# Kernel optimization log

Measured on AMD Instinct MI355X. Metric: run time of the kernel, lower is better.

The kernel has to match this reference:

```python
import jax, jax.numpy as jnp
import numpy as np

N = 100_000      # nodes
E = 500_000      # bonds
DN = 128         # dim_node_embedding
DB = 64          # dim_bond_embedding
NTOK = 4         # num_bond_token
DIN = 2 * DN + 2 * DB  # 384
LEAKY = 0.001
LN_EPS = 1e-5
DIST_MAX = 20.0
STEP = 0.5


def _lrelu(v):
    return jnp.where(v >= 0, v, LEAKY * v)


def _layernorm(v, w, b):
    m = v.mean(-1, keepdims=True)
    var = ((v - m) ** 2).mean(-1, keepdims=True)
    return (v - m) / jnp.sqrt(var + LN_EPS) * w + b


def setup_inputs() -> dict:
    key = jax.random.key(0)
    ks = jax.random.split(key, 20)
    x = jax.random.normal(ks[0], (N, 3), dtype=jnp.float32) * 3.0
    pos = jax.random.normal(ks[1], (N, 3), dtype=jnp.float32)
    node_embedding = jax.random.normal(ks[2], (N, DN), dtype=jnp.float32)
    i0 = jax.random.randint(ks[3], (E,), 0, N)
    off = jax.random.randint(ks[4], (E,), 1, N)  # nonzero -> no self-bonds
    bond_index = jnp.stack([i0, (i0 + off) % N], axis=1).astype(jnp.int32)
    bond_types = jax.random.randint(ks[5], (E,), 0, NTOK).astype(jnp.int32)
    s = 0.02
    params = dict(
        bond_emb=jax.random.normal(ks[6], (NTOK, DB), dtype=jnp.float32),
        W0=jax.random.normal(ks[7], (DIN, DN), dtype=jnp.float32) * s,
        b0=jnp.zeros((DN,), jnp.float32),
        W1=jax.random.normal(ks[8], (DN, DN), dtype=jnp.float32) * s,
        b1=jnp.zeros((DN,), jnp.float32),
        ln1_w=jnp.ones((DN,), jnp.float32),
        ln1_b=jnp.zeros((DN,), jnp.float32),
        W2=jax.random.normal(ks[9], (DN, DN), dtype=jnp.float32) * s,
        b2=jnp.zeros((DN,), jnp.float32),
        ln2_w=jnp.ones((DN,), jnp.float32),
        ln2_b=jnp.zeros((DN,), jnp.float32),
        Wo=jax.random.normal(ks[10], (DN, 2), dtype=jnp.float32) * s,
        bo=jnp.zeros((2,), jnp.float32),
    )
    return dict(x=x, pos=pos, node_embedding=node_embedding,
                bond_index=bond_index, bond_types=bond_types, **params)


def reference(x, pos, node_embedding, bond_index, bond_types,
              bond_emb, W0, b0, W1, b1, ln1_w, ln1_b,
              W2, b2, ln2_w, ln2_b, Wo, bo):
    i = bond_index[:, 0]
    j = bond_index[:, 1]

    # ---- BondLength geometry ----
    diff = x[i] - x[j]                                   # [E,3]
    dist = jnp.linalg.norm(diff, axis=-1, keepdims=True)  # [E,1]
    u = diff / dist                                       # [E,3] unit j->i? (i-j)/d
    direction = jnp.stack([u, -u], axis=-1)               # [E,3,2]

    # ---- Smearing (gaussian RBF + overflow bin, normalized) ----
    offset = jnp.linspace(0.0, DIST_MAX, DB - 1, dtype=jnp.float32)  # [63]
    delta = DIST_MAX / (DB - 2)
    coeff = -0.5 / (delta * delta)
    rbf = jnp.exp(coeff * (dist - offset) ** 2)            # [E,63]
    ovf = (dist >= DIST_MAX).astype(x.dtype)               # [E,1]
    smear = jnp.concatenate([rbf, ovf], axis=-1)           # [E,64]
    smear = smear / smear.sum(axis=-1, keepdims=True)

    # ---- Edge MLP (LeakyMLP, num_layer=2, dim_end=2) ----
    feat = jnp.concatenate(
        [node_embedding[i], node_embedding[j], bond_emb[bond_types], smear],
        axis=-1)                                           # [E,384]
    h = _lrelu(feat @ W0 + b0)
    h = _lrelu(_layernorm(h @ W1 + b1, ln1_w, ln1_b))
    h = _lrelu(_layernorm(h @ W2 + b2, ln2_w, ln2_b))
    force = h @ Wo + bo                                    # [E,2]

    # ---- position update (scatter-add) ----
    update = force[:, None, :] * direction                 # [E,3,2]
    pos = pos.at[i].add(STEP * update[..., 0])
    pos = pos.at[j].add(STEP * update[..., 1])
    return pos
```

## Files before the change

### kernel.cpp

```cpp
#include <hip/hip_runtime.h>
#include <stdint.h>

#define N_EDGES 500000
#define N_NODES 100000
#define PREP_NG 2
#define TBINS 1280

typedef __attribute__((ext_vector_type(8))) short short8;
typedef __attribute__((ext_vector_type(4))) float floatx4;

__device__ __forceinline__ uint16_t f2bf(float f) {
  union { float f; uint32_t u; } cv; cv.f = f;
  uint32_t u = cv.u;
  return (uint16_t)((u + 0x7FFFu + ((u >> 16) & 1u)) >> 16);
}
__device__ __forceinline__ uint32_t pk2bf(float lo, float hi) {
  return __builtin_amdgcn_perm(__float_as_uint(hi), __float_as_uint(lo), 0x07060302u);
}
__device__ __forceinline__ uint16_t bftrunc(float f) {
  return (uint16_t)(__float_as_uint(f) >> 16);
}
__device__ __forceinline__ float bf2f_lo(uint32_t u) { return __uint_as_float(u << 16); }
__device__ __forceinline__ float bf2f_hi(uint32_t u) { return __uint_as_float(u & 0xFFFF0000u); }
__device__ __forceinline__ float lrelu(float v) { return fmaxf(v, 0.001f * v); }

__global__ void prep0_kernel(const float* __restrict__ W0, const float* __restrict__ b0,
                             const float* __restrict__ W1, const float* __restrict__ W2,
                             const float* __restrict__ bemb,
                             uint16_t* __restrict__ w0ab, uint16_t* __restrict__ w1f,
                             uint16_t* __restrict__ w2f, float* __restrict__ be0f,
                             const float* __restrict__ pos, float* __restrict__ out, int npos) {
  int id = blockIdx.x * 256 + threadIdx.x;
  if (id < 32768) {
    int f = id;
    int j = f & 7, lane = (f >> 3) & 63, ntt = (f >> 9) & 15, ks = f >> 13;
    int k = ks * 32 + (lane >> 4) * 8 + j;
    int row = (ntt < 8) ? k : (128 + k);
    int col = (ntt & 7) * 16 + (lane & 15);
    w0ab[f] = f2bf(W0[row * 128 + col]);
  } else if (id < 49152) {
    int f = id - 32768;
    int j = f & 7, lane = (f >> 3) & 63, nt = (f >> 9) & 7, ks = f >> 12;
    int k = ks * 32 + (lane >> 4) * 8 + j;
    w1f[f] = f2bf(W1[k * 128 + nt * 16 + (lane & 15)]);
  } else if (id < 65536) {
    int f = id - 49152;
    int j = f & 7, lane = (f >> 3) & 63, nt = (f >> 9) & 7, ks = f >> 12;
    int k = ks * 32 + (lane >> 4) * 8 + j;
    w2f[f] = f2bf(W2[k * 128 + nt * 16 + (lane & 15)]);
  } else if (id < 66048) {
    int t = id - 65536; int ty = t >> 7, n = t & 127;
    float s = b0[n];
    for (int kk = 0; kk < 64; ++kk) s += bemb[ty * 64 + kk] * W0[(256 + kk) * 128 + n];
    be0f[t] = s;
  } else if (id - 66048 < npos) {
    out[id - 66048] = pos[id - 66048];
  }
}

__global__ void prep_t_kernel(const float* __restrict__ W0, const float* __restrict__ be0f,
                              uint16_t* __restrict__ T) {
  int id = blockIdx.x * 256 + threadIdx.x;
  if (id >= 4 * TBINS * 128) return;
  int n = id & 127;
  int tb = id >> 7;
  int b = tb % TBINS;
  int ty = tb / TBINS;
  float dist = (float)b * (1.0f / 32.0f);
  const float delta = 20.0f / 62.0f;
  const float coeff = -0.5f / (delta * delta);
  float sum = 0.0f;
  for (int k = 0; k < 63; ++k) { float d = dist - (float)k * delta; sum += __expf(coeff * d * d); }
  float ovf = (dist >= 20.0f) ? 1.0f : 0.0f;
  sum += ovf;
  float rs = 1.0f / sum;
  float s = be0f[ty * 128 + n];
  for (int k = 0; k < 63; ++k) {
    float d = dist - (float)k * delta;
    s += __expf(coeff * d * d) * rs * W0[(320 + k) * 128 + n];
  }
  s += ovf * rs * W0[(320 + 63) * 128 + n];
  T[id] = f2bf(s);
}

__global__ __attribute__((amdgpu_flat_work_group_size(256, 256), amdgpu_waves_per_eu(1, 4)))
void prep_p_kernel(const float* __restrict__ nemb, const uint16_t* __restrict__ w0ab,
                   uint16_t* __restrict__ Pa, uint16_t* __restrict__ Pb) {
  __shared__ __align__(16) uint16_t aLds[4 * PREP_NG * 16 * 136];
  const int tid = threadIdx.x;
  const int lane = tid & 63;
  const int wave = tid >> 6;
  const int n15 = lane & 15;
  const int quad = lane >> 4;
  uint16_t* myA = aLds + wave * (PREP_NG * 16 * 136);
  const int base = blockIdx.x * (64 * PREP_NG) + wave * (16 * PREP_NG);

  {
    const int le = lane >> 2, sub = lane & 3;
#pragma unroll
    for (int it = 0; it < PREP_NG; ++it) {
      int r = base + it * 16 + le; if (r >= N_NODES) r = N_NODES - 1;
      const float4* src = (const float4*)(nemb + (size_t)r * 128);
#pragma unroll
      for (int g = 0; g < 4; ++g) {
        float4 a = src[sub * 8 + g * 2], b = src[sub * 8 + g * 2 + 1];
        uint4 pk;
        pk.x = pk2bf(a.x, a.y); pk.y = pk2bf(a.z, a.w);
        pk.z = pk2bf(b.x, b.y); pk.w = pk2bf(b.z, b.w);
        *(uint4*)(myA + (it * 16 + le) * 136 + sub * 32 + g * 8) = pk;
      }
    }
  }

  const short8* wfv = (const short8*)w0ab + lane;
#pragma unroll
  for (int q = 0; q < 4; ++q) {
    short8 bfr[16];
#pragma unroll
    for (int ks = 0; ks < 4; ++ks)
#pragma unroll
      for (int nq = 0; nq < 4; ++nq)
        bfr[ks * 4 + nq] = wfv[(ks * 16 + q * 4 + nq) * 64];
#pragma unroll
    for (int it = 0; it < PREP_NG; ++it) {
      floatx4 acc[4];
#pragma unroll
      for (int nq = 0; nq < 4; ++nq) acc[nq] = (floatx4){0.f, 0.f, 0.f, 0.f};
#pragma unroll
      for (int ks = 0; ks < 4; ++ks) {
        short8 a = *(const short8*)(myA + (it * 16 + n15) * 136 + ks * 32 + quad * 8);
#pragma unroll
        for (int nq = 0; nq < 4; ++nq)
          acc[nq] = __builtin_amdgcn_mfma_f32_16x16x32_bf16(a, bfr[ks * 4 + nq], acc[nq], 0, 0, 0);
      }
      uint16_t* dst = (q < 2) ? Pa : Pb;
      int cbase = ((q & 1) * 4) * 16 + n15;
#pragma unroll
      for (int nq = 0; nq < 4; ++nq) {
        int c = cbase + nq * 16;
#pragma unroll
        for (int r = 0; r < 4; ++r) {
          int row = base + it * 16 + quad * 4 + r;
          if (row < N_NODES) dst[(size_t)row * 128 + c] = bftrunc(acc[nq][r]);
        }
      }
    }
  }
}

template <int NKS>
__device__ __forceinline__ void gemm2(const uint16_t* __restrict__ wf,
                                      const uint16_t* aR0, const uint16_t* aR1,
                                      int lane, floatx4* acc0, floatx4* acc1) {
  const short8* wfv = (const short8*)wf + lane;
  short8 a0[NKS], a1[NKS];
#pragma unroll
  for (int ks = 0; ks < NKS; ++ks) {
    a0[ks] = *(const short8*)(aR0 + ks * 32);
    a1[ks] = *(const short8*)(aR1 + ks * 32);
  }
#pragma unroll
  for (int ks = 0; ks < NKS; ++ks)
#pragma unroll
    for (int nt = 0; nt < 8; ++nt) {
      short8 b = wfv[(ks * 8 + nt) * 64];
      acc0[nt] = __builtin_amdgcn_mfma_f32_16x16x32_bf16(a0[ks], b, acc0[nt], 0, 0, 0);
      acc1[nt] = __builtin_amdgcn_mfma_f32_16x16x32_bf16(a1[ks], b, acc1[nt], 0, 0, 0);
    }
}

__global__ __attribute__((amdgpu_flat_work_group_size(256, 256)))
void bond_mlp_kernel(const float* __restrict__ x,
                     const int* __restrict__ bidx, const int* __restrict__ btyp,
                     const uint16_t* __restrict__ Pa, const uint16_t* __restrict__ Pb,
                     const uint16_t* __restrict__ Tt, const uint16_t* __restrict__ w1f,
                     const uint16_t* __restrict__ w2f,
                     const float* __restrict__ b1, const float* __restrict__ ln1w,
                     const float* __restrict__ ln1b,
                     const float* __restrict__ b2, const float* __restrict__ ln2w,
                     const float* __restrict__ ln2b,
                     const float* __restrict__ Wo, const float* __restrict__ bo,
                     float* __restrict__ out) {
  __shared__ __align__(16) uint16_t hA_all[4 * 32 * 136];
  __shared__ float u_lds[128][3];
  __shared__ int ij_lds[128][2];

  const int tid = threadIdx.x;
  const int lane = tid & 63;
  const int wave = tid >> 6;
  const int n15 = lane & 15;
  const int quad = lane >> 4;

  uint16_t* hA = hA_all + wave * (32 * 136);

#pragma unroll
  for (int p = 0; p < 2; ++p) {
    const int le = lane >> 2, sub = lane & 3;
    const int row = p * 16 + le;
    const int gr = wave * 32 + row;
    const int ge = blockIdx.x * 128 + gr;
    const bool valid = ge < N_EDGES;
    int vi = 0, vj = 0, bt = 0;
    if (valid) { vi = bidx[2 * ge]; vj = bidx[2 * ge + 1]; bt = btyp[ge]; }
    float dx, dy, dz;
    if (valid) {
      dx = x[3 * vi]     - x[3 * vj];
      dy = x[3 * vi + 1] - x[3 * vj + 1];
      dz = x[3 * vi + 2] - x[3 * vj + 2];
    } else { dx = 1.0f; dy = 0.0f; dz = 0.0f; }
    float dist = sqrtf(dx * dx + dy * dy + dz * dz);
    float rinv = 1.0f / dist;
    if (sub == 0) {
      u_lds[gr][0] = dx * rinv; u_lds[gr][1] = dy * rinv; u_lds[gr][2] = dz * rinv;
      ij_lds[gr][0] = vi; ij_lds[gr][1] = vj;
    }
    float fb = fminf(dist, 39.5f) * 32.0f;
    int bi = (int)fb;
    float w = fb - (float)bi;
    const uint4* pa = (const uint4*)(Pa + (size_t)vi * 128 + sub * 32);
    const uint4* pb = (const uint4*)(Pb + (size_t)vj * 128 + sub * 32);
    const uint16_t* trow = Tt + ((size_t)(bt * TBINS + bi)) * 128 + sub * 32;
    const uint4* t0p = (const uint4*)trow;
    const uint4* t1p = (const uint4*)(trow + 128);
#pragma unroll
    for (int g = 0; g < 4; ++g) {
      uint4 av = pa[g], bv = pb[g], t0 = t0p[g], t1 = t1p[g];
      uint4 pk;
      {
        float lo = bf2f_lo(av.x) + bf2f_lo(bv.x), hi = bf2f_hi(av.x) + bf2f_hi(bv.x);
        float l0 = bf2f_lo(t0.x), l1 = bf2f_lo(t1.x), h0 = bf2f_hi(t0.x), h1 = bf2f_hi(t1.x);
        pk.x = pk2bf(lrelu(lo + l0 + w * (l1 - l0)), lrelu(hi + h0 + w * (h1 - h0)));
      }
      {
        float lo = bf2f_lo(av.y) + bf2f_lo(bv.y), hi = bf2f_hi(av.y) + bf2f_hi(bv.y);
        float l0 = bf2f_lo(t0.y), l1 = bf2f_lo(t1.y), h0 = bf2f_hi(t0.y), h1 = bf2f_hi(t1.y);
        pk.y = pk2bf(lrelu(lo + l0 + w * (l1 - l0)), lrelu(hi + h0 + w * (h1 - h0)));
      }
      {
        float lo = bf2f_lo(av.z) + bf2f_lo(bv.z), hi = bf2f_hi(av.z) + bf2f_hi(bv.z);
        float l0 = bf2f_lo(t0.z), l1 = bf2f_lo(t1.z), h0 = bf2f_hi(t0.z), h1 = bf2f_hi(t1.z);
        pk.z = pk2bf(lrelu(lo + l0 + w * (l1 - l0)), lrelu(hi + h0 + w * (h1 - h0)));
      }
      {
        float lo = bf2f_lo(av.w) + bf2f_lo(bv.w), hi = bf2f_hi(av.w) + bf2f_hi(bv.w);
        float l0 = bf2f_lo(t0.w), l1 = bf2f_lo(t1.w), h0 = bf2f_hi(t0.w), h1 = bf2f_hi(t1.w);
        pk.w = pk2bf(lrelu(lo + l0 + w * (l1 - l0)), lrelu(hi + h0 + w * (h1 - h0)));
      }
      *(uint4*)(hA + row * 136 + sub * 32 + g * 8) = pk;
    }
  }

  const uint16_t* aR0 = hA + n15 * 136 + quad * 8;
  const uint16_t* aR1 = hA + (16 + n15) * 136 + quad * 8;

  floatx4 acc0[8], acc1[8];
#pragma unroll
  for (int nt = 0; nt < 8; ++nt) {
    acc0[nt] = (floatx4){0.f, 0.f, 0.f, 0.f};
    acc1[nt] = (floatx4){0.f, 0.f, 0.f, 0.f};
  }
  gemm2<4>(w1f, aR0, aR1, lane, acc0, acc1);

  {
    float bv[8], wv[8], bb2[8];
#pragma unroll
    for (int nt = 0; nt < 8; ++nt) {
      int col = nt * 16 + n15;
      bv[nt] = b1[col]; wv[nt] = ln1w[col]; bb2[nt] = ln1b[col];
    }
#pragma unroll
    for (int t = 0; t < 2; ++t) {
      floatx4* acc = t ? acc1 : acc0;
      float s[4] = {0,0,0,0}, q[4] = {0,0,0,0};
#pragma unroll
      for (int nt = 0; nt < 8; ++nt)
#pragma unroll
        for (int r = 0; r < 4; ++r) { float v = acc[nt][r] + bv[nt]; s[r] += v; q[r] += v * v; }
#pragma unroll
      for (int m = 1; m <= 8; m <<= 1)
#pragma unroll
        for (int r = 0; r < 4; ++r) { s[r] += __shfl_xor(s[r], m); q[r] += __shfl_xor(q[r], m); }
      float mean[4], rstd[4];
#pragma unroll
      for (int r = 0; r < 4; ++r) {
        mean[r] = s[r] * (1.0f / 128.0f);
        float var = q[r] * (1.0f / 128.0f) - mean[r] * mean[r];
        rstd[r] = rsqrtf(var + 1e-5f);
      }
#pragma unroll
      for (int nt = 0; nt < 8; ++nt)
#pragma unroll
        for (int r = 0; r < 4; ++r) {
          float v = acc[nt][r] + bv[nt];
          float vn = (v - mean[r]) * rstd[r] * wv[nt] + bb2[nt];
          hA[(t * 16 + quad * 4 + r) * 136 + nt * 16 + n15] = bftrunc(lrelu(vn));
        }
    }
  }

#pragma unroll
  for (int nt = 0; nt < 8; ++nt) {
    acc0[nt] = (floatx4){0.f, 0.f, 0.f, 0.f};
    acc1[nt] = (floatx4){0.f, 0.f, 0.f, 0.f};
  }
  gemm2<4>(w2f, aR0, aR1, lane, acc0, acc1);

  {
    float bv[8], wv[8], bb2[8], wo0[8], wo1[8];
#pragma unroll
    for (int nt = 0; nt < 8; ++nt) {
      int col = nt * 16 + n15;
      bv[nt] = b2[col]; wv[nt] = ln2w[col]; bb2[nt] = ln2b[col];
      wo0[nt] = Wo[2 * col]; wo1[nt] = Wo[2 * col + 1];
    }
    float bo0 = bo[0], bo1 = bo[1];
#pragma unroll
    for (int t = 0; t < 2; ++t) {
      floatx4* acc = t ? acc1 : acc0;
      float s[4] = {0,0,0,0}, q[4] = {0,0,0,0};
#pragma unroll
      for (int nt = 0; nt < 8; ++nt)
#pragma unroll
        for (int r = 0; r < 4; ++r) { float v = acc[nt][r] + bv[nt]; s[r] += v; q[r] += v * v; }
#pragma unroll
      for (int m = 1; m <= 8; m <<= 1)
#pragma unroll
        for (int r = 0; r < 4; ++r) { s[r] += __shfl_xor(s[r], m); q[r] += __shfl_xor(q[r], m); }
      float mean[4], rstd[4];
#pragma unroll
      for (int r = 0; r < 4; ++r) {
        mean[r] = s[r] * (1.0f / 128.0f);
        float var = q[r] * (1.0f / 128.0f) - mean[r] * mean[r];
        rstd[r] = rsqrtf(var + 1e-5f);
      }
      float f0[4] = {0,0,0,0}, f1[4] = {0,0,0,0};
#pragma unroll
      for (int nt = 0; nt < 8; ++nt)
#pragma unroll
        for (int r = 0; r < 4; ++r) {
          float v = acc[nt][r] + bv[nt];
          float vn = lrelu((v - mean[r]) * rstd[r] * wv[nt] + bb2[nt]);
          f0[r] += vn * wo0[nt];
          f1[r] += vn * wo1[nt];
        }
#pragma unroll
      for (int m = 1; m <= 8; m <<= 1)
#pragma unroll
        for (int r = 0; r < 4; ++r) { f0[r] += __shfl_xor(f0[r], m); f1[r] += __shfl_xor(f1[r], m); }

      if (n15 < 4) {
        int gr = wave * 32 + t * 16 + quad * 4 + n15;
        int ge2 = blockIdx.x * 128 + gr;
        if (ge2 < N_EDGES) {
          float F0 = (n15 == 0) ? f0[0] : (n15 == 1) ? f0[1] : (n15 == 2) ? f0[2] : f0[3];
          float F1 = (n15 == 0) ? f1[0] : (n15 == 1) ? f1[1] : (n15 == 2) ? f1[2] : f1[3];
          F0 += bo0; F1 += bo1;
          float ux = u_lds[gr][0], uy = u_lds[gr][1], uz = u_lds[gr][2];
          int ii = ij_lds[gr][0], jj = ij_lds[gr][1];
          float c0 = 0.5f * F0;
          float c1 = -0.5f * F1;
          atomicAdd(out + 3 * ii,     c0 * ux);
          atomicAdd(out + 3 * ii + 1, c0 * uy);
          atomicAdd(out + 3 * ii + 2, c0 * uz);
          atomicAdd(out + 3 * jj,     c1 * ux);
          atomicAdd(out + 3 * jj + 1, c1 * uy);
          atomicAdd(out + 3 * jj + 2, c1 * uz);
        }
      }
    }
  }
}

extern "C" void kernel_launch(void* const* d_in, const int* in_sizes, int n_in,
                              void* d_out, int out_size, void* d_ws, size_t ws_size,
                              hipStream_t stream) {
  const float* x    = (const float*)d_in[0];
  const float* pos  = (const float*)d_in[1];
  const float* nemb = (const float*)d_in[2];
  const int*   bidx = (const int*)d_in[3];
  const int*   btyp = (const int*)d_in[4];
  const float* bemb = (const float*)d_in[5];
  const float* W0   = (const float*)d_in[6];
  const float* b0   = (const float*)d_in[7];
  const float* W1   = (const float*)d_in[8];
  const float* b1   = (const float*)d_in[9];
  const float* ln1w = (const float*)d_in[10];
  const float* ln1b = (const float*)d_in[11];
  const float* W2   = (const float*)d_in[12];
  const float* b2   = (const float*)d_in[13];
  const float* ln2w = (const float*)d_in[14];
  const float* ln2b = (const float*)d_in[15];
  const float* Wo   = (const float*)d_in[16];
  const float* bo   = (const float*)d_in[17];
  float* out = (float*)d_out;

  uint16_t* w0ab = (uint16_t*)d_ws;
  uint16_t* w1f  = w0ab + 32768;
  uint16_t* w2f  = w1f + 16384;
  float*    be0f = (float*)(w2f + 16384);
  uint16_t* Tt   = (uint16_t*)(be0f + 512);
  uint16_t* Pa   = Tt + 4 * TBINS * 128;
  uint16_t* Pb   = Pa + (size_t)N_NODES * 128;

  prep0_kernel<<<(66048 + out_size + 255) / 256, 256, 0, stream>>>(
      W0, b0, W1, W2, bemb, w0ab, w1f, w2f, be0f, pos, out, out_size);
  prep_t_kernel<<<(4 * TBINS * 128 + 255) / 256, 256, 0, stream>>>(W0, be0f, Tt);
  prep_p_kernel<<<(N_NODES + 64 * PREP_NG - 1) / (64 * PREP_NG), 256, 0, stream>>>(
      nemb, w0ab, Pa, Pb);
  bond_mlp_kernel<<<(N_EDGES + 127) / 128, 256, 0, stream>>>(
      x, bidx, btyp, Pa, Pb, Tt, w1f, w2f,
      b1, ln1w, ln1b, b2, ln2w, ln2b, Wo, bo, out);
}
```

Measured before the change: 407.6 us.

## Stage MLP weights in LDS via global_load_lds and halve edges per block

The bond MLP kernel now loads the W1 and W2 bf16 fragments into shared memory with direct global-to-LDS loads and reads MFMA B operands from LDS instead of global memory. Each block now handles 64 edges, so each wave computes one 16-row tile instead of two, and block-wide barriers are added around the staging. prep_t is restructured so each block computes the RBF values for one distance bin once in shared memory and reuses them across the 512 outputs. The trade-off is more blocks, more barriers, a 32 KB LDS buffer that may lower occupancy, and less reuse of each weight fragment per load.

```diff
diff --git a/kernel.cpp b/kernel.cpp
--- a/kernel.cpp
+++ b/kernel.cpp
@@ -23,6 +23,12 @@
 __device__ __forceinline__ float bf2f_lo(uint32_t u) { return __uint_as_float(u << 16); }
 __device__ __forceinline__ float bf2f_hi(uint32_t u) { return __uint_as_float(u & 0xFFFF0000u); }
 __device__ __forceinline__ float lrelu(float v) { return fmaxf(v, 0.001f * v); }
+
+__device__ __forceinline__ void gload_lds16(const uint16_t* g, uint16_t* l) {
+  __builtin_amdgcn_global_load_lds(
+      (const __attribute__((address_space(1))) void*)g,
+      (__attribute__((address_space(3))) void*)l, 16, 0, 0);
+}
 
 __global__ void prep0_kernel(const float* __restrict__ W0, const float* __restrict__ b0,
                              const float* __restrict__ W1, const float* __restrict__ W2,
@@ -60,27 +66,28 @@
 
 __global__ void prep_t_kernel(const float* __restrict__ W0, const float* __restrict__ be0f,
                               uint16_t* __restrict__ T) {
-  int id = blockIdx.x * 256 + threadIdx.x;
-  if (id >= 4 * TBINS * 128) return;
-  int n = id & 127;
-  int tb = id >> 7;
-  int b = tb % TBINS;
-  int ty = tb / TBINS;
+  __shared__ float rbf[64];
+  int b = blockIdx.x;
+  int t = threadIdx.x;
   float dist = (float)b * (1.0f / 32.0f);
   const float delta = 20.0f / 62.0f;
   const float coeff = -0.5f / (delta * delta);
+  if (t < 64) {
+    float v;
+    if (t < 63) { float d = dist - (float)t * delta; v = __expf(coeff * d * d); }
+    else v = (dist >= 20.0f) ? 1.0f : 0.0f;
+    rbf[t] = v;
+  }
+  __syncthreads();
   float sum = 0.0f;
-  for (int k = 0; k < 63; ++k) { float d = dist - (float)k * delta; sum += __expf(coeff * d * d); }
-  float ovf = (dist >= 20.0f) ? 1.0f : 0.0f;
-  sum += ovf;
+  for (int k = 0; k < 64; ++k) sum += rbf[k];
   float rs = 1.0f / sum;
-  float s = be0f[ty * 128 + n];
-  for (int k = 0; k < 63; ++k) {
-    float d = dist - (float)k * delta;
-    s += __expf(coeff * d * d) * rs * W0[(320 + k) * 128 + n];
-  }
-  s += ovf * rs * W0[(320 + 63) * 128 + n];
-  T[id] = f2bf(s);
+  for (int o = t; o < 512; o += 256) {
+    int ty = o >> 7, n = o & 127;
+    float s = be0f[ty * 128 + n];
+    for (int k = 0; k < 64; ++k) s += rbf[k] * rs * W0[(320 + k) * 128 + n];
+    T[((size_t)(ty * TBINS + b)) * 128 + n] = f2bf(s);
+  }
 }
 
 __global__ __attribute__((amdgpu_flat_work_group_size(256, 256), amdgpu_waves_per_eu(1, 4)))
@@ -148,24 +155,17 @@
   }
 }
 
-template <int NKS>
-__device__ __forceinline__ void gemm2(const uint16_t* __restrict__ wf,
-                                      const uint16_t* aR0, const uint16_t* aR1,
-                                      int lane, floatx4* acc0, floatx4* acc1) {
-  const short8* wfv = (const short8*)wf + lane;
-  short8 a0[NKS], a1[NKS];
-#pragma unroll
-  for (int ks = 0; ks < NKS; ++ks) {
-    a0[ks] = *(const short8*)(aR0 + ks * 32);
-    a1[ks] = *(const short8*)(aR1 + ks * 32);
-  }
-#pragma unroll
-  for (int ks = 0; ks < NKS; ++ks)
+__device__ __forceinline__ void gemm_lds(const uint16_t* ws, const uint16_t* aRow,
+                                         int lane, floatx4* acc) {
+  short8 a[4];
+#pragma unroll
+  for (int ks = 0; ks < 4; ++ks) a[ks] = *(const short8*)(aRow + ks * 32);
+#pragma unroll
+  for (int ks = 0; ks < 4; ++ks)
 #pragma unroll
     for (int nt = 0; nt < 8; ++nt) {
-      short8 b = wfv[(ks * 8 + nt) * 64];
-      acc0[nt] = __builtin_amdgcn_mfma_f32_16x16x32_bf16(a0[ks], b, acc0[nt], 0, 0, 0);
-      acc1[nt] = __builtin_amdgcn_mfma_f32_16x16x32_bf16(a1[ks], b, acc1[nt], 0, 0, 0);
+      short8 b = *(const short8*)(ws + (ks * 8 + nt) * 512 + lane * 8);
+      acc[nt] = __builtin_amdgcn_mfma_f32_16x16x32_bf16(a[ks], b, acc[nt], 0, 0, 0);
     }
 }
 
@@ -181,9 +181,10 @@
                      const float* __restrict__ ln2b,
                      const float* __restrict__ Wo, const float* __restrict__ bo,
                      float* __restrict__ out) {
-  __shared__ __align__(16) uint16_t hA_all[4 * 32 * 136];
-  __shared__ float u_lds[128][3];
-  __shared__ int ij_lds[128][2];
+  __shared__ __align__(16) uint16_t wstage[16384];
+  __shared__ __align__(16) uint16_t hA_all[4 * 16 * 136];
+  __shared__ float u_lds[64][3];
+  __shared__ int ij_lds[64][2];
 
   const int tid = threadIdx.x;
   const int lane = tid & 63;
@@ -191,14 +192,16 @@
   const int n15 = lane & 15;
   const int quad = lane >> 4;
 
-  uint16_t* hA = hA_all + wave * (32 * 136);
-
-#pragma unroll
-  for (int p = 0; p < 2; ++p) {
+  uint16_t* hA = hA_all + wave * (16 * 136);
+
+#pragma unroll
+  for (int j = 0; j < 8; ++j)
+    gload_lds16(w1f + (wave * 8 + j) * 512 + lane * 8, wstage + (wave * 8 + j) * 512);
+
+  {
     const int le = lane >> 2, sub = lane & 3;
-    const int row = p * 16 + le;
-    const int gr = wave * 32 + row;
-    const int ge = blockIdx.x * 128 + gr;
+    const int gr = wave * 16 + le;
+    const int ge = blockIdx.x * 64 + gr;
     const bool valid = ge < N_EDGES;
     int vi = 0, vj = 0, bt = 0;
     if (valid) { vi = bidx[2 * ge]; vj = bidx[2 * ge + 1]; bt = btyp[ge]; }
@@ -246,20 +249,22 @@
         float l0 = bf2f_lo(t0.w), l1 = bf2f_lo(t1.w), h0 = bf2f_hi(t0.w), h1 = bf2f_hi(t1.w);
         pk.w = pk2bf(lrelu(lo + l0 + w * (l1 - l0)), lrelu(hi + h0 + w * (h1 - h0)));
       }
-      *(uint4*)(hA + row * 136 + sub * 32 + g * 8) = pk;
-    }
-  }
-
-  const uint16_t* aR0 = hA + n15 * 136 + quad * 8;
-  const uint16_t* aR1 = hA + (16 + n15) * 136 + quad * 8;
-
-  floatx4 acc0[8], acc1[8];
-#pragma unroll
-  for (int nt = 0; nt < 8; ++nt) {
-    acc0[nt] = (floatx4){0.f, 0.f, 0.f, 0.f};
-    acc1[nt] = (floatx4){0.f, 0.f, 0.f, 0.f};
-  }
-  gemm2<4>(w1f, aR0, aR1, lane, acc0, acc1);
+      *(uint4*)(hA + le * 136 + sub * 32 + g * 8) = pk;
+    }
+  }
+  __syncthreads();
+
+  const uint16_t* aRow = hA + n15 * 136 + quad * 8;
+
+  floatx4 acc[8];
+#pragma unroll
+  for (int nt = 0; nt < 8; ++nt) acc[nt] = (floatx4){0.f, 0.f, 0.f, 0.f};
+  gemm_lds(wstage, aRow, lane, acc);
+
+  __syncthreads();
+#pragma unroll
+  for (int j = 0; j < 8; ++j)
+    gload_lds16(w2f + (wave * 8 + j) * 512 + lane * 8, wstage + (wave * 8 + j) * 512);
 
   {
     float bv[8], wv[8], bb2[8];
@@ -268,42 +273,36 @@
       int col = nt * 16 + n15;
       bv[nt] = b1[col]; wv[nt] = ln1w[col]; bb2[nt] = ln1b[col];
     }
-#pragma unroll
-    for (int t = 0; t < 2; ++t) {
-      floatx4* acc = t ? acc1 : acc0;
-      float s[4] = {0,0,0,0}, q[4] = {0,0,0,0};
-#pragma unroll
-      for (int nt = 0; nt < 8; ++nt)
-#pragma unroll
-        for (int r = 0; r < 4; ++r) { float v = acc[nt][r] + bv[nt]; s[r] += v; q[r] += v * v; }
-#pragma unroll
-      for (int m = 1; m <= 8; m <<= 1)
-#pragma unroll
-        for (int r = 0; r < 4; ++r) { s[r] += __shfl_xor(s[r], m); q[r] += __shfl_xor(q[r], m); }
-      float mean[4], rstd[4];
+    float s[4] = {0,0,0,0}, q[4] = {0,0,0,0};
+#pragma unroll
+    for (int nt = 0; nt < 8; ++nt)
+#pragma unroll
+      for (int r = 0; r < 4; ++r) { float v = acc[nt][r] + bv[nt]; s[r] += v; q[r] += v * v; }
+#pragma unroll
+    for (int m = 1; m <= 8; m <<= 1)
+#pragma unroll
+      for (int r = 0; r < 4; ++r) { s[r] += __shfl_xor(s[r], m); q[r] += __shfl_xor(q[r], m); }
+    float mean[4], rstd[4];
+#pragma unroll
+    for (int r = 0; r < 4; ++r) {
+      mean[r] = s[r] * (1.0f / 128.0f);
+      float var = q[r] * (1.0f / 128.0f) - mean[r] * mean[r];
+      rstd[r] = rsqrtf(var + 1e-5f);
+    }
+#pragma unroll
+    for (int nt = 0; nt < 8; ++nt)
 #pragma unroll
       for (int r = 0; r < 4; ++r) {
-        mean[r] = s[r] * (1.0f / 128.0f);
-        float var = q[r] * (1.0f / 128.0f) - mean[r] * mean[r];
-        rstd[r] = rsqrtf(var + 1e-5f);
-      }
-#pragma unroll
-      for (int nt = 0; nt < 8; ++nt)
-#pragma unroll
-        for (int r = 0; r < 4; ++r) {
-          float v = acc[nt][r] + bv[nt];
-          float vn = (v - mean[r]) * rstd[r] * wv[nt] + bb2[nt];
-          hA[(t * 16 + quad * 4 + r) * 136 + nt * 16 + n15] = bftrunc(lrelu(vn));
-        }
-    }
-  }
-
-#pragma unroll
-  for (int nt = 0; nt < 8; ++nt) {
-    acc0[nt] = (floatx4){0.f, 0.f, 0.f, 0.f};
-    acc1[nt] = (floatx4){0.f, 0.f, 0.f, 0.f};
-  }
-  gemm2<4>(w2f, aR0, aR1, lane, acc0, acc1);
+        float v = acc[nt][r] + bv[nt];
+        float vn = (v - mean[r]) * rstd[r] * wv[nt] + bb2[nt];
+        hA[(quad * 4 + r) * 136 + nt * 16 + n15] = bftrunc(lrelu(vn));
+      }
+  }
+  __syncthreads();
+
+#pragma unroll
+  for (int nt = 0; nt < 8; ++nt) acc[nt] = (floatx4){0.f, 0.f, 0.f, 0.f};
+  gemm_lds(wstage, aRow, lane, acc);
 
   {
     float bv[8], wv[8], bb2[8], wo0[8], wo1[8];
@@ -313,59 +312,54 @@
       bv[nt] = b2[col]; wv[nt] = ln2w[col]; bb2[nt] = ln2b[col];
       wo0[nt] = Wo[2 * col]; wo1[nt] = Wo[2 * col + 1];
     }
-    float bo0 = bo[0], bo1 = bo[1];
-#pragma unroll
-    for (int t = 0; t < 2; ++t) {
-      floatx4* acc = t ? acc1 : acc0;
-      float s[4] = {0,0,0,0}, q[4] = {0,0,0,0};
-#pragma unroll
-      for (int nt = 0; nt < 8; ++nt)
-#pragma unroll
-        for (int r = 0; r < 4; ++r) { float v = acc[nt][r] + bv[nt]; s[r] += v; q[r] += v * v; }
-#pragma unroll
-      for (int m = 1; m <= 8; m <<= 1)
-#pragma unroll
-        for (int r = 0; r < 4; ++r) { s[r] += __shfl_xor(s[r], m); q[r] += __shfl_xor(q[r], m); }
-      float mean[4], rstd[4];
+    float s[4] = {0,0,0,0}, q[4] = {0,0,0,0};
+#pragma unroll
+    for (int nt = 0; nt < 8; ++nt)
+#pragma unroll
+      for (int r = 0; r < 4; ++r) { float v = acc[nt][r] + bv[nt]; s[r] += v; q[r] += v * v; }
+#pragma unroll
+    for (int m = 1; m <= 8; m <<= 1)
+#pragma unroll
+      for (int r = 0; r < 4; ++r) { s[r] += __shfl_xor(s[r], m); q[r] += __shfl_xor(q[r], m); }
+    float mean[4], rstd[4];
+#pragma unroll
+    for (int r = 0; r < 4; ++r) {
+      mean[r] = s[r] * (1.0f / 128.0f);
+      float var = q[r] * (1.0f / 128.0f) - mean[r] * mean[r];
+      rstd[r] = rsqrtf(var + 1e-5f);
+    }
+    float f0[4] = {0,0,0,0}, f1[4] = {0,0,0,0};
+#pragma unroll
+    for (int nt = 0; nt < 8; ++nt)
 #pragma unroll
       for (int r = 0; r < 4; ++r) {
-        mean[r] = s[r] * (1.0f / 128.0f);
-        float var = q[r] * (1.0f / 128.0f) - mean[r] * mean[r];
-        rstd[r] = rsqrtf(var + 1e-5f);
-      }
-      float f0[4] = {0,0,0,0}, f1[4] = {0,0,0,0};
-#pragma unroll
-      for (int nt = 0; nt < 8; ++nt)
-#pragma unroll
-        for (int r = 0; r < 4; ++r) {
-          float v = acc[nt][r] + bv[nt];
-          float vn = lrelu((v - mean[r]) * rstd[r] * wv[nt] + bb2[nt]);
-          f0[r] += vn * wo0[nt];
-          f1[r] += vn * wo1[nt];
-        }
-#pragma unroll
-      for (int m = 1; m <= 8; m <<= 1)
-#pragma unroll
-        for (int r = 0; r < 4; ++r) { f0[r] += __shfl_xor(f0[r], m); f1[r] += __shfl_xor(f1[r], m); }
-
-      if (n15 < 4) {
-        int gr = wave * 32 + t * 16 + quad * 4 + n15;
-        int ge2 = blockIdx.x * 128 + gr;
-        if (ge2 < N_EDGES) {
-          float F0 = (n15 == 0) ? f0[0] : (n15 == 1) ? f0[1] : (n15 == 2) ? f0[2] : f0[3];
-          float F1 = (n15 == 0) ? f1[0] : (n15 == 1) ? f1[1] : (n15 == 2) ? f1[2] : f1[3];
-          F0 += bo0; F1 += bo1;
-          float ux = u_lds[gr][0], uy = u_lds[gr][1], uz = u_lds[gr][2];
-          int ii = ij_lds[gr][0], jj = ij_lds[gr][1];
-          float c0 = 0.5f * F0;
-          float c1 = -0.5f * F1;
-          atomicAdd(out + 3 * ii,     c0 * ux);
-          atomicAdd(out + 3 * ii + 1, c0 * uy);
-          atomicAdd(out + 3 * ii + 2, c0 * uz);
-          atomicAdd(out + 3 * jj,     c1 * ux);
-          atomicAdd(out + 3 * jj + 1, c1 * uy);
-          atomicAdd(out + 3 * jj + 2, c1 * uz);
-        }
+        float v = acc[nt][r] + bv[nt];
+        float vn = lrelu((v - mean[r]) * rstd[r] * wv[nt] + bb2[nt]);
+        f0[r] += vn * wo0[nt];
+        f1[r] += vn * wo1[nt];
+      }
+#pragma unroll
+    for (int m = 1; m <= 8; m <<= 1)
+#pragma unroll
+      for (int r = 0; r < 4; ++r) { f0[r] += __shfl_xor(f0[r], m); f1[r] += __shfl_xor(f1[r], m); }
+
+    if (n15 < 4) {
+      int gr = wave * 16 + quad * 4 + n15;
+      int ge2 = blockIdx.x * 64 + gr;
+      if (ge2 < N_EDGES) {
+        float F0 = (n15 == 0) ? f0[0] : (n15 == 1) ? f0[1] : (n15 == 2) ? f0[2] : f0[3];
+        float F1 = (n15 == 0) ? f1[0] : (n15 == 1) ? f1[1] : (n15 == 2) ? f1[2] : f1[3];
+        F0 += bo[0]; F1 += bo[1];
+        float ux = u_lds[gr][0], uy = u_lds[gr][1], uz = u_lds[gr][2];
+        int ii = ij_lds[gr][0], jj = ij_lds[gr][1];
+        float c0 = 0.5f * F0;
+        float c1 = -0.5f * F1;
+        atomicAdd(out + 3 * ii,     c0 * ux);
+        atomicAdd(out + 3 * ii + 1, c0 * uy);
+        atomicAdd(out + 3 * ii + 2, c0 * uz);
+        atomicAdd(out + 3 * jj,     c1 * ux);
+        atomicAdd(out + 3 * jj + 1, c1 * uy);
+        atomicAdd(out + 3 * jj + 2, c1 * uz);
       }
     }
   }
@@ -404,10 +398,10 @@
 
   prep0_kernel<<<(66048 + out_size + 255) / 256, 256, 0, stream>>>(
       W0, b0, W1, W2, bemb, w0ab, w1f, w2f, be0f, pos, out, out_size);
-  prep_t_kernel<<<(4 * TBINS * 128 + 255) / 256, 256, 0, stream>>>(W0, be0f, Tt);
+  prep_t_kernel<<<TBINS, 256, 0, stream>>>(W0, be0f, Tt);
   prep_p_kernel<<<(N_NODES + 64 * PREP_NG - 1) / (64 * PREP_NG), 256, 0, stream>>>(
       nemb, w0ab, Pa, Pb);
-  bond_mlp_kernel<<<(N_EDGES + 127) / 128, 256, 0, stream>>>(
+  bond_mlp_kernel<<<(N_EDGES + 63) / 64, 256, 0, stream>>>(
       x, bidx, btyp, Pa, Pb, Tt, w1f, w2f,
       b1, ln1w, ln1b, b2, ln2w, ln2b, Wo, bo, out);
 }
```

New measurement: 352.3 us. -13.6%, faster.
